# Optimization experiments

Hardware: AMD Instinct MI355X
Metric: run time of the kernel (lower is better)

Reference implementation:

```python
import jax, jax.numpy as jnp
import numpy as np
from jax import lax

# Quantization bit-widths per the module: QuantAct(16) on input,
# QuantConv2d(precision[0]=8), QuantAct(precision[0]+3=11) after relu1,
# QuantLinear(precision[1]=8).
INPUT_BIT = 16
CONV_W_BIT = 8
RELU_BIT = 11
DENSE_W_BIT = 8
EPS = 1e-8


def round_ste(x):
    # straight-through estimator rounding (HAWQ SymmetricQuantFunction)
    return x + lax.stop_gradient(jnp.round(x) - x)


def quant_act(x, bit):
    """Per-tensor symmetric dynamic activation quantization (HAWQ QuantAct).
    Returns fake-quantized x and its scaling factor."""
    n = 2 ** (bit - 1) - 1
    scale = lax.stop_gradient(jnp.maximum(jnp.max(jnp.abs(x)), EPS) / n)
    x_q = jnp.clip(round_ste(x / scale), -n, n) * scale
    return x_q, scale


def quant_weight(w, bit):
    """Per-output-channel symmetric weight quantization. w: [out, ...].
    Returns integer-valued weights and per-channel scale [out]."""
    n = 2 ** (bit - 1) - 1
    absmax = jnp.max(jnp.abs(w.reshape(w.shape[0], -1)), axis=1)
    sf = lax.stop_gradient(jnp.maximum(absmax, EPS) / n)
    bshape = (w.shape[0],) + (1,) * (w.ndim - 1)
    w_int = jnp.clip(round_ste(w / sf.reshape(bshape)), -n, n)
    return w_int, sf


def quant_conv2d(x, p_sf, w, b, bit, stride, pad):
    w_int, w_sf = quant_weight(w, bit)          # [O,I,kh,kw], [O]
    x_int = x / p_sf                            # integer-valued activations
    out_int = lax.conv_general_dilated(
        x_int, w_int, window_strides=(stride, stride),
        padding=((pad, pad), (pad, pad)),
        dimension_numbers=("NCHW", "OIHW", "NCHW"))
    bias_sf = p_sf * w_sf                       # [O]
    b_int = round_ste(b / bias_sf)
    out = (out_int + b_int[None, :, None, None]) * bias_sf[None, :, None, None]
    return out, w_sf


def quant_linear(x, p_sf, w, b, bit):
    w_int, w_sf = quant_weight(w, bit)          # [O,I], [O]
    x_int = x / p_sf
    bias_sf = p_sf * w_sf                       # [O]
    b_int = round_ste(b / bias_sf)
    out = (jnp.einsum("bi,oi->bo", x_int, w_int) + b_int[None, :]) * bias_sf[None, :]
    return out


def setup_inputs() -> dict:
    key = jax.random.key(0)
    k1, k2, k3, k4, k5 = jax.random.split(key, 5)
    B, Cin, H, W = 256, 3, 64, 64
    Cout, K = 64, 3
    Fin, Fout = Cout * 32 * 32, 256  # stride-2 conv -> 32x32 spatial
    x = jax.random.normal(k1, (B, Cin, H, W), dtype=jnp.float32)
    conv_w = jax.random.normal(k2, (Cout, Cin, K, K), dtype=jnp.float32) * 0.1
    conv_b = jax.random.normal(k3, (Cout,), dtype=jnp.float32) * 0.01
    dense_w = jax.random.normal(k4, (Fout, Fin), dtype=jnp.float32) * 0.02
    dense_b = jax.random.normal(k5, (Fout,), dtype=jnp.float32) * 0.01
    return {"x": x, "conv_w": conv_w, "conv_b": conv_b,
            "dense_w": dense_w, "dense_b": dense_b}


def reference(x, conv_w, conv_b, dense_w, dense_b):
    # x, p_sf = quant_input(x)
    xq, p_sf = quant_act(x, INPUT_BIT)
    # x, w_sf = conv(x, p_sf)
    h, w_sf = quant_conv2d(xq, p_sf, conv_w, conv_b, CONV_W_BIT, stride=2, pad=1)
    # relu1
    h = jax.nn.relu(h)
    # x, p_sf = quant_relu(x, p_sf, w_sf)  (requantize at relu_bit)
    h, p_sf = quant_act(h, RELU_BIT)
    # flatten
    h = h.reshape(h.shape[0], -1)
    # relu2(enc_dense(x, p_sf))
    out = jax.nn.relu(quant_linear(h, p_sf, dense_w, dense_b, DENSE_W_BIT))
    return out
```

## Files before the change

kernel.cpp:

```cpp
#include <hip/hip_runtime.h>
#include <hip/hip_fp16.h>
#include <cstdint>

#define B_   256
#define CIN  3
#define HW_  64
#define COUT 64
#define FIN  65536
#define FOUT 256

#define ACC_F    0
#define SC_F     65536
#define WSF2_F   65552
#define CBSF_F   65808
#define CBINT_F  65872
#define CWINT_F  65936
#define H16_BYTE (512*1024)

typedef _Float16 half8  __attribute__((ext_vector_type(8)));
typedef _Float16 half4v __attribute__((ext_vector_type(4)));
typedef float    floatx4 __attribute__((ext_vector_type(4)));
typedef unsigned short u16;

__device__ inline float blockMax(float v) {
    #pragma unroll
    for (int off = 32; off; off >>= 1) v = fmaxf(v, __shfl_down(v, off));
    __shared__ float sm[8];
    const int lane = threadIdx.x & 63, w = threadIdx.x >> 6;
    if (lane == 0) sm[w] = v;
    __syncthreads();
    float m = sm[0];
    const int nw = blockDim.x >> 6;
    for (int i = 1; i < nw; i++) m = fmaxf(m, sm[i]);
    return m;
}

__global__ void k_amax_x(const float* __restrict__ x, unsigned* __restrict__ tgt, int n4) {
    const float4* x4 = (const float4*)x;
    float m = 0.f;
    for (int i = blockIdx.x * blockDim.x + threadIdx.x; i < n4; i += gridDim.x * blockDim.x) {
        float4 v = x4[i];
        m = fmaxf(m, fmaxf(fmaxf(fabsf(v.x), fabsf(v.y)), fmaxf(fabsf(v.z), fabsf(v.w))));
    }
    float bm = blockMax(m);
    if (threadIdx.x == 0) atomicMax(tgt, __float_as_uint(bm));
}

__global__ void k_wamax(const float* __restrict__ dw, unsigned* __restrict__ wabs) {
    const int row = blockIdx.x >> 2;
    const int q   = blockIdx.x & 3;
    const float4* r = (const float4*)(dw + (size_t)row * FIN) + q * 4096;
    float m = 0.f;
    for (int i = threadIdx.x; i < 4096; i += 256) {
        float4 v = r[i];
        m = fmaxf(m, fmaxf(fmaxf(fabsf(v.x), fabsf(v.y)), fmaxf(fabsf(v.z), fabsf(v.w))));
    }
    float bm = blockMax(m);
    if (threadIdx.x == 0) atomicMax(wabs + row, __float_as_uint(bm));
}

__global__ void k_qconvw(const float* __restrict__ cw, const float* __restrict__ cb,
                         float* ws) {
    const int o = threadIdx.x;
    const float maxx = __uint_as_float(((const unsigned*)ws)[SC_F + 0]);
    const float p_sf = fmaxf(maxx, 1e-8f) / 32767.0f;
    if (o == 0) ws[SC_F + 2] = p_sf;
    float wv[27];
    float m = 0.f;
    #pragma unroll
    for (int i = 0; i < 27; i++) { wv[i] = cw[o * 27 + i]; m = fmaxf(m, fabsf(wv[i])); }
    const float sf = fmaxf(m, 1e-8f) / 127.0f;
    #pragma unroll
    for (int i = 0; i < 27; i++) {
        float qv = fminf(127.f, fmaxf(-127.f, rintf(wv[i] / sf)));
        ws[CWINT_F + o * 27 + i] = qv;
    }
    const float bsf = p_sf * sf;
    ws[CBSF_F + o]  = bsf;
    ws[CBINT_F + o] = rintf(cb[o] / bsf);
}

__global__ __launch_bounds__(256) void k_conv(const float* __restrict__ x,
                                              const float* __restrict__ ws,
                                              u16* __restrict__ h16,
                                              unsigned* __restrict__ maxh) {
    const int b   = blockIdx.x >> 3;
    const int oyt = (blockIdx.x & 7) * 4;
    const int t   = threadIdx.x;
    const int ox  = t & 31;
    const int ch  = __builtin_amdgcn_readfirstlane((t >> 6) & 1);
    const int oy  = oyt + ((t >> 7) << 1) + ((t >> 5) & 1);
    const float p_sf  = ws[SC_F + 2];
    const float inv_p = 1.0f / p_sf;
    const float* xb = x + (size_t)b * (CIN * HW_ * HW_);

    float xs[27];
    #pragma unroll
    for (int ci = 0; ci < 3; ci++)
        #pragma unroll
        for (int ky = 0; ky < 3; ky++) {
            const int iy = 2 * oy - 1 + ky;
            const bool yok = ((unsigned)iy < 64u);
            #pragma unroll
            for (int kx = 0; kx < 3; kx++) {
                const int ix = 2 * ox - 1 + kx;
                float v = (yok && ((unsigned)ix < 64u)) ? xb[(ci * HW_ + iy) * HW_ + ix] : 0.f;
                float q = rintf(v * inv_p);
                xs[ci * 9 + ky * 3 + kx] = fminf(32767.f, fmaxf(-32767.f, q));
            }
        }

    float acc[32];
    const float* wr = ws + CWINT_F + ch * (32 * 27);
    #pragma unroll
    for (int c = 0; c < 32; c++) {
        float a = 0.f;
        #pragma unroll
        for (int k = 0; k < 27; k++) a = fmaf(xs[k], wr[c * 27 + k], a);
        acc[c] = a;
    }

    float mx = 0.f;
    const size_t base = (size_t)b * FIN + (size_t)ch * 32 * 1024 + oy * 32 + ox;
    #pragma unroll
    for (int c = 0; c < 32; c++) {
        const int co = ch * 32 + c;
        float h = (acc[c] + ws[CBINT_F + co]) * ws[CBSF_F + co];
        h = fmaxf(h, 0.f);
        mx = fmaxf(mx, h);
        h16[base + (size_t)c * 1024] = __half_as_ushort(__float2half(h));
    }
    float bm = blockMax(mx);
    if (t == 0) atomicMax(maxh, __float_as_uint(bm));
}

__global__ __launch_bounds__(256) void k_gemm(const u16* __restrict__ h16,
                                              const float* __restrict__ dw,
                                              const float* __restrict__ ws,
                                              float* __restrict__ accb) {
    __shared__ __align__(16) _Float16 As[128][72];
    __shared__ __align__(16) _Float16 Bs[128][72];
    __shared__ float invB[128];

    const int tid = threadIdx.x;
    const int tm  = (blockIdx.x >> 1) * 128;
    const int tn  = (blockIdx.x & 1) * 128;
    const int k0  = blockIdx.y * 1024;

    const float max_h  = __uint_as_float(((const unsigned*)ws)[SC_F + 1]);
    const float p2     = fmaxf(max_h, 1e-8f) / 1023.0f;
    const float inv_p2 = 1.0f / p2;

    if (tid < 128) {
        float am = fmaxf(__uint_as_float(((const unsigned*)ws)[WSF2_F + tn + tid]), 1e-8f);
        invB[tid] = 127.0f / am;
    }

    floatx4 acc[4][4];
    const floatx4 zz = {0.f, 0.f, 0.f, 0.f};
    #pragma unroll
    for (int i = 0; i < 4; i++)
        #pragma unroll
        for (int j = 0; j < 4; j++) acc[i][j] = zz;

    const int wv = tid >> 6, lane = tid & 63;
    const int wm = (wv >> 1) * 64, wn = (wv & 1) * 64;
    const int lm = lane & 15, quad = lane >> 4;

    for (int kk = 0; kk < 16; kk++) {
        __syncthreads();
        #pragma unroll
        for (int r = 0; r < 4; r++) {
            const int i = tid + r * 256;
            const int row = i >> 3, c = i & 7;
            const u16* p = h16 + (size_t)(tm + row) * FIN + k0 + kk * 64 + c * 8;
            half8 hv = *(const half8*)p;
            half8 qv;
            #pragma unroll
            for (int j = 0; j < 8; j++) {
                float f = (float)hv[j];
                qv[j] = (_Float16)fminf(1023.f, rintf(f * inv_p2));
            }
            *(half8*)&As[row][c * 8] = qv;
        }
        #pragma unroll
        for (int r = 0; r < 8; r++) {
            const int i = tid + r * 256;
            const int row = i >> 4, c = i & 15;
            const float* p = dw + (size_t)(tn + row) * FIN + k0 + kk * 64 + c * 4;
            float4 v = *(const float4*)p;
            const float is = invB[row];
            half4v qv;
            qv[0] = (_Float16)fminf(127.f, fmaxf(-127.f, rintf(v.x * is)));
            qv[1] = (_Float16)fminf(127.f, fmaxf(-127.f, rintf(v.y * is)));
            qv[2] = (_Float16)fminf(127.f, fmaxf(-127.f, rintf(v.z * is)));
            qv[3] = (_Float16)fminf(127.f, fmaxf(-127.f, rintf(v.w * is)));
            *(half4v*)&Bs[row][c * 4] = qv;
        }
        __syncthreads();
        #pragma unroll
        for (int ks = 0; ks < 2; ks++) {
            half8 af[4], bf[4];
            #pragma unroll
            for (int mi = 0; mi < 4; mi++)
                af[mi] = *(const half8*)&As[wm + mi * 16 + lm][ks * 32 + quad * 8];
            #pragma unroll
            for (int ni = 0; ni < 4; ni++)
                bf[ni] = *(const half8*)&Bs[wn + ni * 16 + lm][ks * 32 + quad * 8];
            #pragma unroll
            for (int mi = 0; mi < 4; mi++)
                #pragma unroll
                for (int ni = 0; ni < 4; ni++)
                    acc[mi][ni] = __builtin_amdgcn_mfma_f32_16x16x32_f16(af[mi], bf[ni], acc[mi][ni], 0, 0, 0);
        }
    }

    #pragma unroll
    for (int mi = 0; mi < 4; mi++)
        #pragma unroll
        for (int ni = 0; ni < 4; ni++)
            #pragma unroll
            for (int r = 0; r < 4; r++) {
                const int row = tm + wm + mi * 16 + quad * 4 + r;
                const int col = tn + wn + ni * 16 + lm;
                atomicAdd(accb + row * FOUT + col, acc[mi][ni][r]);
            }
}

__global__ void k_epi(const float* __restrict__ accb, const float* __restrict__ db,
                      const float* __restrict__ ws, float* __restrict__ out) {
    const int idx = blockIdx.x * 256 + threadIdx.x;
    const int n = idx & 255;
    const float max_h = __uint_as_float(((const unsigned*)ws)[SC_F + 1]);
    const float p2 = fmaxf(max_h, 1e-8f) / 1023.0f;
    const float am = fmaxf(__uint_as_float(((const unsigned*)ws)[WSF2_F + n]), 1e-8f);
    const float wsf = am / 127.0f;
    const float bsf = p2 * wsf;
    const float bint = rintf(db[n] / bsf);
    out[idx] = fmaxf(0.f, (accb[idx] + bint) * bsf);
}

extern "C" void kernel_launch(void* const* d_in, const int* in_sizes, int n_in,
                              void* d_out, int out_size, void* d_ws, size_t ws_size,
                              hipStream_t stream) {
    (void)in_sizes; (void)n_in; (void)out_size; (void)ws_size;
    const float* x  = (const float*)d_in[0];
    const float* cw = (const float*)d_in[1];
    const float* cb = (const float*)d_in[2];
    const float* dw = (const float*)d_in[3];
    const float* db = (const float*)d_in[4];
    float* out = (float*)d_out;
    float* ws  = (float*)d_ws;
    u16* h16   = (u16*)((char*)d_ws + H16_BYTE);
    float* accb = ws + ACC_F;
    unsigned* scal = (unsigned*)(ws + SC_F);
    unsigned* wabs = (unsigned*)(ws + WSF2_F);

    hipMemsetAsync(d_ws, 0, (size_t)(65536 + 16 + 256) * sizeof(float), stream);

    k_amax_x<<<512, 256, 0, stream>>>(x, scal + 0, (B_ * CIN * HW_ * HW_) / 4);
    k_wamax<<<1024, 256, 0, stream>>>(dw, wabs);
    k_qconvw<<<1, 64, 0, stream>>>(cw, cb, ws);
    k_conv<<<2048, 256, 0, stream>>>(x, ws, h16, scal + 1);
    k_gemm<<<dim3(4, 64), 256, 0, stream>>>(h16, dw, ws, accb);
    k_epi<<<256, 256, 0, stream>>>(accb, db, ws, out);
}
```

Baseline: 207.6 us.

## Fuse all stages into one persistent kernel with grid barriers

Replaces the six kernel launches and the large memset with a single 512-block persistent kernel that separates the phases (absmax, conv, GEMM, reduction/epilogue) with software grid barriers built on atomic counters. The GEMM switches from atomicAdd accumulation to per-block partial tiles reduced deterministically in a final phase, register-prefetches the next K tile, and does quantization rounding in packed fp16 using magic-number adds. This removes launch gaps and atomic traffic, but it relies on all 512 blocks being co-resident, which the grid barrier needs to avoid deadlock. It also adds about 33 MB of partial-sum traffic and the fp16 rounding tricks could differ from the float rintf rounding.

```diff
diff --git a/kernel.cpp b/kernel.cpp
--- a/kernel.cpp
+++ b/kernel.cpp
@@ -2,242 +2,280 @@
 #include <hip/hip_fp16.h>
 #include <cstdint>
 
-#define B_   256
-#define CIN  3
-#define HW_  64
-#define COUT 64
 #define FIN  65536
-#define FOUT 256
-
-#define ACC_F    0
-#define SC_F     65536
-#define WSF2_F   65552
-#define CBSF_F   65808
-#define CBINT_F  65872
-#define CWINT_F  65936
-#define H16_BYTE (512*1024)
-
-typedef _Float16 half8  __attribute__((ext_vector_type(8)));
-typedef _Float16 half4v __attribute__((ext_vector_type(4)));
+#define NBLK 512
+
+#define CNT_F   0
+#define SPART_F 64
+#define WABS_F  320
+#define SFW_F   576
+#define WINT_F  640
+#define HPART_F 2368
+#define H16_B   16384
+#define PART_B  33570816
+
+typedef _Float16 half8 __attribute__((ext_vector_type(8)));
+typedef _Float16 half2v __attribute__((ext_vector_type(2)));
 typedef float    floatx4 __attribute__((ext_vector_type(4)));
 typedef unsigned short u16;
 
 __device__ inline float blockMax(float v) {
     #pragma unroll
     for (int off = 32; off; off >>= 1) v = fmaxf(v, __shfl_down(v, off));
-    __shared__ float sm[8];
+    __shared__ float sm[4];
     const int lane = threadIdx.x & 63, w = threadIdx.x >> 6;
     if (lane == 0) sm[w] = v;
     __syncthreads();
-    float m = sm[0];
-    const int nw = blockDim.x >> 6;
-    for (int i = 1; i < nw; i++) m = fmaxf(m, sm[i]);
+    float m = fmaxf(fmaxf(sm[0], sm[1]), fmaxf(sm[2], sm[3]));
+    __syncthreads();
     return m;
 }
 
-__global__ void k_amax_x(const float* __restrict__ x, unsigned* __restrict__ tgt, int n4) {
-    const float4* x4 = (const float4*)x;
-    float m = 0.f;
-    for (int i = blockIdx.x * blockDim.x + threadIdx.x; i < n4; i += gridDim.x * blockDim.x) {
-        float4 v = x4[i];
-        m = fmaxf(m, fmaxf(fmaxf(fabsf(v.x), fabsf(v.y)), fmaxf(fabsf(v.z), fabsf(v.w))));
-    }
-    float bm = blockMax(m);
-    if (threadIdx.x == 0) atomicMax(tgt, __float_as_uint(bm));
-}
-
-__global__ void k_wamax(const float* __restrict__ dw, unsigned* __restrict__ wabs) {
-    const int row = blockIdx.x >> 2;
-    const int q   = blockIdx.x & 3;
-    const float4* r = (const float4*)(dw + (size_t)row * FIN) + q * 4096;
-    float m = 0.f;
-    for (int i = threadIdx.x; i < 4096; i += 256) {
-        float4 v = r[i];
-        m = fmaxf(m, fmaxf(fmaxf(fabsf(v.x), fabsf(v.y)), fmaxf(fabsf(v.z), fabsf(v.w))));
-    }
-    float bm = blockMax(m);
-    if (threadIdx.x == 0) atomicMax(wabs + row, __float_as_uint(bm));
-}
-
-__global__ void k_qconvw(const float* __restrict__ cw, const float* __restrict__ cb,
-                         float* ws) {
-    const int o = threadIdx.x;
-    const float maxx = __uint_as_float(((const unsigned*)ws)[SC_F + 0]);
-    const float p_sf = fmaxf(maxx, 1e-8f) / 32767.0f;
-    if (o == 0) ws[SC_F + 2] = p_sf;
-    float wv[27];
-    float m = 0.f;
-    #pragma unroll
-    for (int i = 0; i < 27; i++) { wv[i] = cw[o * 27 + i]; m = fmaxf(m, fabsf(wv[i])); }
-    const float sf = fmaxf(m, 1e-8f) / 127.0f;
-    #pragma unroll
-    for (int i = 0; i < 27; i++) {
-        float qv = fminf(127.f, fmaxf(-127.f, rintf(wv[i] / sf)));
-        ws[CWINT_F + o * 27 + i] = qv;
-    }
-    const float bsf = p_sf * sf;
-    ws[CBSF_F + o]  = bsf;
-    ws[CBINT_F + o] = rintf(cb[o] / bsf);
-}
-
-__global__ __launch_bounds__(256) void k_conv(const float* __restrict__ x,
-                                              const float* __restrict__ ws,
-                                              u16* __restrict__ h16,
-                                              unsigned* __restrict__ maxh) {
-    const int b   = blockIdx.x >> 3;
-    const int oyt = (blockIdx.x & 7) * 4;
-    const int t   = threadIdx.x;
-    const int ox  = t & 31;
-    const int ch  = __builtin_amdgcn_readfirstlane((t >> 6) & 1);
-    const int oy  = oyt + ((t >> 7) << 1) + ((t >> 5) & 1);
-    const float p_sf  = ws[SC_F + 2];
+__device__ inline void gbar(unsigned* c, unsigned target) {
+    __syncthreads();
+    if (threadIdx.x == 0) {
+        __threadfence();
+        __hip_atomic_fetch_add(c, 1u, __ATOMIC_ACQ_REL, __HIP_MEMORY_SCOPE_AGENT);
+        while (__hip_atomic_load(c, __ATOMIC_ACQUIRE, __HIP_MEMORY_SCOPE_AGENT) < target)
+            __builtin_amdgcn_s_sleep(1);
+        __threadfence();
+    }
+    __syncthreads();
+}
+
+__global__ __launch_bounds__(256, 2) void mega(const float* __restrict__ x,
+                                               const float* __restrict__ cw,
+                                               const float* __restrict__ cb,
+                                               const float* __restrict__ dw,
+                                               const float* __restrict__ db,
+                                               float* __restrict__ out,
+                                               float* __restrict__ ws) {
+    const int b = blockIdx.x, tid = threadIdx.x;
+    unsigned* cnt = (unsigned*)ws;
+
+    __shared__ __align__(16) _Float16 As[128][72];
+    __shared__ __align__(16) _Float16 Bs[64][72];
+    __shared__ float scB[64];
+    __shared__ float bsfL[64], bintL[64];
+    __shared__ float red2[128];
+
+    u16* h16 = (u16*)((char*)ws + H16_B);
+
+    if (b < 256) {
+        const float4* x4 = (const float4*)x;
+        float m = 0.f;
+        #pragma unroll
+        for (int j = 0; j < 12; j++) {
+            float4 v = x4[b * 3072 + j * 256 + tid];
+            m = fmaxf(m, fmaxf(fmaxf(fabsf(v.x), fabsf(v.y)), fmaxf(fabsf(v.z), fabsf(v.w))));
+        }
+        float bm = blockMax(m);
+        if (tid == 0) ws[SPART_F + b] = bm;
+    } else {
+        const int row = b - 256;
+        const float4* r4 = (const float4*)(dw + (size_t)row * FIN);
+        float m = 0.f;
+        for (int j = 0; j < 64; j++) {
+            float4 v = r4[j * 256 + tid];
+            m = fmaxf(m, fmaxf(fmaxf(fabsf(v.x), fabsf(v.y)), fmaxf(fabsf(v.z), fabsf(v.w))));
+        }
+        float bm = blockMax(m);
+        if (tid == 0) ws[WABS_F + row] = bm;
+        if (b == 511 && tid < 64) {
+            float wv[27]; float mm = 0.f;
+            #pragma unroll
+            for (int i = 0; i < 27; i++) { wv[i] = cw[tid * 27 + i]; mm = fmaxf(mm, fabsf(wv[i])); }
+            const float sfw = fmaxf(mm, 1e-8f) / 127.0f;
+            ws[SFW_F + tid] = sfw;
+            #pragma unroll
+            for (int i = 0; i < 27; i++)
+                ws[WINT_F + tid * 27 + i] = fminf(127.f, fmaxf(-127.f, rintf(wv[i] / sfw)));
+        }
+    }
+    gbar(cnt + 0, NBLK);
+
+    const float p_sf = fmaxf(blockMax(ws[SPART_F + tid]), 1e-8f) / 32767.0f;
     const float inv_p = 1.0f / p_sf;
-    const float* xb = x + (size_t)b * (CIN * HW_ * HW_);
-
-    float xs[27];
-    #pragma unroll
-    for (int ci = 0; ci < 3; ci++)
-        #pragma unroll
-        for (int ky = 0; ky < 3; ky++) {
-            const int iy = 2 * oy - 1 + ky;
-            const bool yok = ((unsigned)iy < 64u);
-            #pragma unroll
-            for (int kx = 0; kx < 3; kx++) {
-                const int ix = 2 * ox - 1 + kx;
-                float v = (yok && ((unsigned)ix < 64u)) ? xb[(ci * HW_ + iy) * HW_ + ix] : 0.f;
-                float q = rintf(v * inv_p);
-                xs[ci * 9 + ky * 3 + kx] = fminf(32767.f, fmaxf(-32767.f, q));
+    if (tid < 64) {
+        const float bsf = p_sf * ws[SFW_F + tid];
+        bsfL[tid] = bsf;
+        bintL[tid] = rintf(cb[tid] / bsf);
+    }
+    __syncthreads();
+
+    float mx = 0.f;
+    {
+        const int ox = tid & 31;
+        const int ch = __builtin_amdgcn_readfirstlane((tid >> 6) & 1);
+        const float* wr = ws + WINT_F + ch * 864;
+        #pragma unroll
+        for (int u = 0; u < 4; u++) {
+            const int g = b * 4 + u;
+            const int imgb = g >> 3;
+            const int oy = (g & 7) * 4 + ((tid >> 7) << 1) + ((tid >> 5) & 1);
+            const float* xb = x + (size_t)imgb * (3 * 64 * 64);
+            float xs[27];
+            #pragma unroll
+            for (int ci = 0; ci < 3; ci++)
+                #pragma unroll
+                for (int ky = 0; ky < 3; ky++) {
+                    const int iy = 2 * oy - 1 + ky;
+                    const bool yok = ((unsigned)iy < 64u);
+                    #pragma unroll
+                    for (int kx = 0; kx < 3; kx++) {
+                        const int ix = 2 * ox - 1 + kx;
+                        float v = (yok && ((unsigned)ix < 64u)) ? xb[(ci * 64 + iy) * 64 + ix] : 0.f;
+                        xs[ci * 9 + ky * 3 + kx] = fminf(32767.f, fmaxf(-32767.f, rintf(v * inv_p)));
+                    }
+                }
+            float acc2[32];
+            #pragma unroll
+            for (int c = 0; c < 32; c++) {
+                float a = 0.f;
+                #pragma unroll
+                for (int k = 0; k < 27; k++) a = fmaf(xs[k], wr[c * 27 + k], a);
+                acc2[c] = a;
             }
-        }
-
-    float acc[32];
-    const float* wr = ws + CWINT_F + ch * (32 * 27);
-    #pragma unroll
-    for (int c = 0; c < 32; c++) {
-        float a = 0.f;
-        #pragma unroll
-        for (int k = 0; k < 27; k++) a = fmaf(xs[k], wr[c * 27 + k], a);
-        acc[c] = a;
-    }
-
-    float mx = 0.f;
-    const size_t base = (size_t)b * FIN + (size_t)ch * 32 * 1024 + oy * 32 + ox;
-    #pragma unroll
-    for (int c = 0; c < 32; c++) {
-        const int co = ch * 32 + c;
-        float h = (acc[c] + ws[CBINT_F + co]) * ws[CBSF_F + co];
-        h = fmaxf(h, 0.f);
-        mx = fmaxf(mx, h);
-        h16[base + (size_t)c * 1024] = __half_as_ushort(__float2half(h));
-    }
-    float bm = blockMax(mx);
-    if (t == 0) atomicMax(maxh, __float_as_uint(bm));
-}
-
-__global__ __launch_bounds__(256) void k_gemm(const u16* __restrict__ h16,
-                                              const float* __restrict__ dw,
-                                              const float* __restrict__ ws,
-                                              float* __restrict__ accb) {
-    __shared__ __align__(16) _Float16 As[128][72];
-    __shared__ __align__(16) _Float16 Bs[128][72];
-    __shared__ float invB[128];
-
-    const int tid = threadIdx.x;
-    const int tm  = (blockIdx.x >> 1) * 128;
-    const int tn  = (blockIdx.x & 1) * 128;
-    const int k0  = blockIdx.y * 1024;
-
-    const float max_h  = __uint_as_float(((const unsigned*)ws)[SC_F + 1]);
-    const float p2     = fmaxf(max_h, 1e-8f) / 1023.0f;
-    const float inv_p2 = 1.0f / p2;
-
-    if (tid < 128) {
-        float am = fmaxf(__uint_as_float(((const unsigned*)ws)[WSF2_F + tn + tid]), 1e-8f);
-        invB[tid] = 127.0f / am;
-    }
-
-    floatx4 acc[4][4];
+            const size_t base = (size_t)imgb * FIN + (size_t)ch * 32768 + oy * 32 + ox;
+            #pragma unroll
+            for (int c = 0; c < 32; c++) {
+                const int co = ch * 32 + c;
+                float h = fmaxf((acc2[c] + bintL[co]) * bsfL[co], 0.f);
+                mx = fmaxf(mx, h);
+                h16[base + (size_t)c * 1024] = __half_as_ushort(__float2half(h));
+            }
+        }
+    }
+    {
+        float bm = blockMax(mx);
+        if (tid == 0) ws[HPART_F + b] = bm;
+    }
+    gbar(cnt + 1, NBLK);
+
+    const float max_h = blockMax(fmaxf(ws[HPART_F + tid], ws[HPART_F + 256 + tid]));
+    const float p2 = fmaxf(max_h, 1e-8f) / 1023.0f;
+    const float inv_p2 = 1023.0f / fmaxf(max_h, 1e-8f);
+
+    const int slice = b >> 3, tile = b & 7;
+    const int tm = (tile >> 2) * 128, tn = (tile & 3) * 64;
+    const int k0 = slice * 1024;
+
+    if (tid < 64) scB[tid] = 127.0f / fmaxf(ws[WABS_F + tn + tid], 1e-8f);
+    __syncthreads();
+
+    const _Float16 invh = (_Float16)inv_p2;
+    const half2v inv2  = {invh, invh};
+    const half2v m1024 = {(_Float16)1024.0f, (_Float16)1024.0f};
+    const half2v m1536 = {(_Float16)1536.0f, (_Float16)1536.0f};
+    const half2v c1023 = {(_Float16)1023.0f, (_Float16)1023.0f};
+    const half2v c127  = {(_Float16)127.0f, (_Float16)127.0f};
+    const half2v cn127 = {(_Float16)-127.0f, (_Float16)-127.0f};
+
+    floatx4 acc[4][2];
     const floatx4 zz = {0.f, 0.f, 0.f, 0.f};
     #pragma unroll
-    for (int i = 0; i < 4; i++)
-        #pragma unroll
-        for (int j = 0; j < 4; j++) acc[i][j] = zz;
+    for (int i = 0; i < 4; i++) { acc[i][0] = zz; acc[i][1] = zz; }
 
     const int wv = tid >> 6, lane = tid & 63;
-    const int wm = (wv >> 1) * 64, wn = (wv & 1) * 64;
+    const int wm = (wv >> 1) * 64, wn = (wv & 1) * 32;
     const int lm = lane & 15, quad = lane >> 4;
 
+    const int arow = tid >> 3, ac8 = tid & 7;
+    const int brow = tid >> 4, bc4 = tid & 15;
+
+    half8  Ar[4];
+    float4 Br[4];
+    auto loadA = [&](int kk) {
+        #pragma unroll
+        for (int r = 0; r < 4; r++)
+            Ar[r] = *(const half8*)(h16 + (size_t)(tm + arow + r * 32) * FIN + k0 + kk * 64 + ac8 * 8);
+    };
+    auto loadB = [&](int kk) {
+        #pragma unroll
+        for (int r = 0; r < 4; r++)
+            Br[r] = *(const float4*)(dw + (size_t)(tn + brow + r * 16) * FIN + k0 + kk * 64 + bc4 * 4);
+    };
+    loadA(0); loadB(0);
+
     for (int kk = 0; kk < 16; kk++) {
+        #pragma unroll
+        for (int r = 0; r < 4; r++) {
+            half2v* hp = (half2v*)&Ar[r];
+            half2v q[4];
+            #pragma unroll
+            for (int j = 0; j < 4; j++) {
+                half2v t = __builtin_elementwise_fma(hp[j], inv2, m1024) - m1024;
+                q[j] = __builtin_elementwise_min(t, c1023);
+            }
+            *(half8*)&As[arow + r * 32][ac8 * 8] = *(half8*)q;
+        }
+        #pragma unroll
+        for (int r = 0; r < 4; r++) {
+            const _Float16 ish = (_Float16)scB[brow + r * 16];
+            const half2v is2 = {ish, ish};
+            half2v w01 = {(_Float16)Br[r].x, (_Float16)Br[r].y};
+            half2v w23 = {(_Float16)Br[r].z, (_Float16)Br[r].w};
+            half2v q01 = __builtin_elementwise_fma(w01, is2, m1536) - m1536;
+            half2v q23 = __builtin_elementwise_fma(w23, is2, m1536) - m1536;
+            q01 = __builtin_elementwise_min(__builtin_elementwise_max(q01, cn127), c127);
+            q23 = __builtin_elementwise_min(__builtin_elementwise_max(q23, cn127), c127);
+            half2v* bp = (half2v*)&Bs[brow + r * 16][bc4 * 4];
+            bp[0] = q01; bp[1] = q23;
+        }
         __syncthreads();
-        #pragma unroll
-        for (int r = 0; r < 4; r++) {
-            const int i = tid + r * 256;
-            const int row = i >> 3, c = i & 7;
-            const u16* p = h16 + (size_t)(tm + row) * FIN + k0 + kk * 64 + c * 8;
-            half8 hv = *(const half8*)p;
-            half8 qv;
-            #pragma unroll
-            for (int j = 0; j < 8; j++) {
-                float f = (float)hv[j];
-                qv[j] = (_Float16)fminf(1023.f, rintf(f * inv_p2));
-            }
-            *(half8*)&As[row][c * 8] = qv;
-        }
-        #pragma unroll
-        for (int r = 0; r < 8; r++) {
-            const int i = tid + r * 256;
-            const int row = i >> 4, c = i & 15;
-            const float* p = dw + (size_t)(tn + row) * FIN + k0 + kk * 64 + c * 4;
-            float4 v = *(const float4*)p;
-            const float is = invB[row];
-            half4v qv;
-            qv[0] = (_Float16)fminf(127.f, fmaxf(-127.f, rintf(v.x * is)));
-            qv[1] = (_Float16)fminf(127.f, fmaxf(-127.f, rintf(v.y * is)));
-            qv[2] = (_Float16)fminf(127.f, fmaxf(-127.f, rintf(v.z * is)));
-            qv[3] = (_Float16)fminf(127.f, fmaxf(-127.f, rintf(v.w * is)));
-            *(half4v*)&Bs[row][c * 4] = qv;
-        }
-        __syncthreads();
+        if (kk < 15) { loadA(kk + 1); loadB(kk + 1); }
         #pragma unroll
         for (int ks = 0; ks < 2; ks++) {
-            half8 af[4], bf[4];
+            half8 af[4], bf[2];
             #pragma unroll
             for (int mi = 0; mi < 4; mi++)
                 af[mi] = *(const half8*)&As[wm + mi * 16 + lm][ks * 32 + quad * 8];
             #pragma unroll
-            for (int ni = 0; ni < 4; ni++)
+            for (int ni = 0; ni < 2; ni++)
                 bf[ni] = *(const half8*)&Bs[wn + ni * 16 + lm][ks * 32 + quad * 8];
             #pragma unroll
             for (int mi = 0; mi < 4; mi++)
                 #pragma unroll
-                for (int ni = 0; ni < 4; ni++)
+                for (int ni = 0; ni < 2; ni++)
                     acc[mi][ni] = __builtin_amdgcn_mfma_f32_16x16x32_f16(af[mi], bf[ni], acc[mi][ni], 0, 0, 0);
         }
-    }
-
-    #pragma unroll
-    for (int mi = 0; mi < 4; mi++)
-        #pragma unroll
-        for (int ni = 0; ni < 4; ni++)
-            #pragma unroll
-            for (int r = 0; r < 4; r++) {
-                const int row = tm + wm + mi * 16 + quad * 4 + r;
-                const int col = tn + wn + ni * 16 + lm;
-                atomicAdd(accb + row * FOUT + col, acc[mi][ni][r]);
-            }
-}
-
-__global__ void k_epi(const float* __restrict__ accb, const float* __restrict__ db,
-                      const float* __restrict__ ws, float* __restrict__ out) {
-    const int idx = blockIdx.x * 256 + threadIdx.x;
-    const int n = idx & 255;
-    const float max_h = __uint_as_float(((const unsigned*)ws)[SC_F + 1]);
-    const float p2 = fmaxf(max_h, 1e-8f) / 1023.0f;
-    const float am = fmaxf(__uint_as_float(((const unsigned*)ws)[WSF2_F + n]), 1e-8f);
-    const float wsf = am / 127.0f;
-    const float bsf = p2 * wsf;
-    const float bint = rintf(db[n] / bsf);
-    out[idx] = fmaxf(0.f, (accb[idx] + bint) * bsf);
+        __syncthreads();
+    }
+    {
+        float* part = (float*)((char*)ws + PART_B) + (size_t)b * 8192;
+        #pragma unroll
+        for (int mi = 0; mi < 4; mi++)
+            #pragma unroll
+            for (int ni = 0; ni < 2; ni++)
+                #pragma unroll
+                for (int r = 0; r < 4; r++) {
+                    const int lmrow = wm + mi * 16 + quad * 4 + r;
+                    const int lncol = wn + ni * 16 + lm;
+                    part[lmrow * 64 + lncol] = acc[mi][ni][r];
+                }
+    }
+    gbar(cnt + 2, NBLK);
+
+    {
+        const int o = b * 128 + (tid & 127);
+        const int m = o >> 8, n = o & 255;
+        const int grp = tid >> 7;
+        const int tile4 = (m >> 7) * 4 + (n >> 6);
+        const int loc = (m & 127) * 64 + (n & 63);
+        const float* base = (const float*)((const char*)ws + PART_B) + (size_t)tile4 * 8192 + loc;
+        float s = 0.f;
+        #pragma unroll
+        for (int j = 0; j < 32; j++) s += base[(size_t)(grp * 32 + j) * 65536];
+        if (grp == 1) red2[tid & 127] = s;
+        __syncthreads();
+        if (grp == 0) {
+            const float total = s + red2[tid];
+            const float wsf = fmaxf(ws[WABS_F + n], 1e-8f) / 127.0f;
+            const float bsf = p2 * wsf;
+            const float bint = rintf(db[n] / bsf);
+            out[o] = fmaxf(0.f, (total + bint) * bsf);
+        }
+    }
 }
 
 extern "C" void kernel_launch(void* const* d_in, const int* in_sizes, int n_in,
@@ -251,17 +289,7 @@
     const float* db = (const float*)d_in[4];
     float* out = (float*)d_out;
     float* ws  = (float*)d_ws;
-    u16* h16   = (u16*)((char*)d_ws + H16_BYTE);
-    float* accb = ws + ACC_F;
-    unsigned* scal = (unsigned*)(ws + SC_F);
-    unsigned* wabs = (unsigned*)(ws + WSF2_F);
-
-    hipMemsetAsync(d_ws, 0, (size_t)(65536 + 16 + 256) * sizeof(float), stream);
-
-    k_amax_x<<<512, 256, 0, stream>>>(x, scal + 0, (B_ * CIN * HW_ * HW_) / 4);
-    k_wamax<<<1024, 256, 0, stream>>>(dw, wabs);
-    k_qconvw<<<1, 64, 0, stream>>>(cw, cb, ws);
-    k_conv<<<2048, 256, 0, stream>>>(x, ws, h16, scal + 1);
-    k_gemm<<<dim3(4, 64), 256, 0, stream>>>(h16, dw, ws, accb);
-    k_epi<<<256, 256, 0, stream>>>(accb, db, ws, out);
-}
+
+    (void)hipMemsetAsync(d_ws, 0, 256, stream);
+    mega<<<NBLK, 256, 0, stream>>>(x, cw, cb, dw, db, out, ws);
+}
```

Result: slower. 515.4 us (+148.3%).
